# Kernel optimization log

Measured on AMD Instinct MI355X. Metric: run time of the kernel, lower is better.

Reference implementation:

```python
import jax, jax.numpy as jnp
import numpy as np

NUM_NODES = 100000
NUM_REL = 500
D = 400          # entity_out_dim[0] * nheads_GAT[0] = 200 * 2
C = 50           # conv_out_channels
B = 16384        # batch of triples


def setup_inputs() -> dict:
    key = jax.random.key(0)
    k = jax.random.split(key, 7)
    entity_emb = jax.random.normal(k[0], (NUM_NODES, D), jnp.float32)
    relation_emb = jax.random.normal(k[1], (NUM_REL, D), jnp.float32)
    # Conv2d(1, C, (1, 3)) weight: [C, 1, 1, 3]; xavier-ish scale
    conv_w = jax.random.normal(k[2], (C, 1, 1, 3), jnp.float32) * 0.5
    conv_b = jnp.zeros((C,), jnp.float32)
    # Linear(D*C, 1)
    fc_w = jax.random.normal(k[3], (1, D * C), jnp.float32) * 0.01
    fc_b = jnp.zeros((1,), jnp.float32)
    heads = jax.random.randint(k[4], (B,), 0, NUM_NODES)
    rels = jax.random.randint(k[5], (B,), 0, NUM_REL)
    tails = jax.random.randint(k[6], (B,), 0, NUM_NODES)
    batch_inputs = jnp.stack([heads, rels, tails], axis=1)  # [B, 3]
    return {
        "entity_emb": entity_emb,
        "relation_emb": relation_emb,
        "conv_w": conv_w,
        "conv_b": conv_b,
        "fc_w": fc_w,
        "fc_b": fc_b,
        "batch_inputs": batch_inputs,
    }


def reference(entity_emb, relation_emb, conv_w, conv_b, fc_w, fc_b, batch_inputs):
    # Gather (h, r, t) rows: irregular access into large tables
    h = entity_emb[batch_inputs[:, 0]]    # [B, D]
    r = relation_emb[batch_inputs[:, 1]]  # [B, D]
    t = entity_emb[batch_inputs[:, 2]]    # [B, D]
    # torch: cat -> [B, 3, D], transpose -> [B, D, 3], unsqueeze -> [B, 1, D, 3]
    x = jnp.stack([h, r, t], axis=-1)     # [B, D, 3]
    # Conv2d(1, C, (1, 3)): kernel spans full width -> per-channel dot over 3
    w = conv_w[:, 0, 0, :]                # [C, 3]
    out = jnp.einsum("bdk,ck->bcd", x, w) + conv_b[None, :, None]  # [B, C, D]
    out = jax.nn.relu(out)                # dropout is identity in eval mode
    # squeeze(-1).view(B, -1): channel-major flatten -> [B, C*D]
    flat = out.reshape(out.shape[0], -1)
    return flat @ fc_w.T + fc_b           # [B, 1]
```

## Files before the change

### kernel.cpp

```cpp
#include <hip/hip_runtime.h>


typedef _Float16 h2 __attribute__((ext_vector_type(2)));
typedef _Float16 h8 __attribute__((ext_vector_type(8)));

constexpr int D    = 400;
constexpr int CP   = 25;
constexpr int DPAD = 404;

static __device__ __forceinline__ float dot2acc(h2 a, h2 b, float c) {
#if __has_builtin(__builtin_amdgcn_fdot2)
    return __builtin_amdgcn_fdot2(a, b, c, false);
#else
    h2 p = a * b; return c + (float)p[0] + (float)p[1];
#endif
}
static __device__ __forceinline__ h2 dup(float v) {
    _Float16 x = (_Float16)v; h2 r; r[0] = x; r[1] = x; return r;
}

__global__ __attribute__((amdgpu_flat_work_group_size(512, 512), amdgpu_waves_per_eu(2, 4)))
void grcnet_pk16f(
    const float* __restrict__ entity_emb,
    const float* __restrict__ relation_emb,
    const float* __restrict__ conv_w,
    const float* __restrict__ conv_b,
    const float* __restrict__ fc_w,
    const float* __restrict__ fc_b,
    const int*   __restrict__ batch_inputs,
    float* __restrict__ out,
    int nB)
{
    __shared__ h2    fc_lds[CP][DPAD];
    __shared__ h2    conv_lds[CP][4];
    __shared__ float partials[2][4][4];

    const int tid  = threadIdx.x;
    const int lane = tid & 63;
    const int wv   = tid >> 6;
    const int grp  = wv >> 1;
    const int hc   = wv & 1;
    const int b0   = blockIdx.x * 16;
    if (b0 >= nB) return;

    const int bbase = __builtin_amdgcn_readfirstlane(b0 + 4 * grp);
    const int* bi = batch_inputs + 3 * bbase;
    const float* p0h = entity_emb   + (size_t)bi[0]  * D + lane;
    const float* p0r = relation_emb + (size_t)bi[1]  * D + lane;
    const float* p0t = entity_emb   + (size_t)bi[2]  * D + lane;
    const float* p1h = entity_emb   + (size_t)bi[3]  * D + lane;
    const float* p1r = relation_emb + (size_t)bi[4]  * D + lane;
    const float* p1t = entity_emb   + (size_t)bi[5]  * D + lane;
    const float* p2h = entity_emb   + (size_t)bi[6]  * D + lane;
    const float* p2r = relation_emb + (size_t)bi[7]  * D + lane;
    const float* p2t = entity_emb   + (size_t)bi[8]  * D + lane;
    const float* p3h = entity_emb   + (size_t)bi[9]  * D + lane;
    const float* p3r = relation_emb + (size_t)bi[10] * D + lane;
    const float* p3t = entity_emb   + (size_t)bi[11] * D + lane;

    const int  d6  = lane + 384;
    const bool a6  = (d6 < D);
    const int  i6  = a6 ? 384 : -lane;
    const h2*  fcb  = (const h2*)fc_lds + lane;
    const h2*  fcb6 = (const h2*)fc_lds + (a6 ? d6 : D);

    #define LOADI(S, IDX)                                                         \
        f##S##_0h = p0h[IDX]; f##S##_0r = p0r[IDX]; f##S##_0t = p0t[IDX];         \
        f##S##_1h = p1h[IDX]; f##S##_1r = p1r[IDX]; f##S##_1t = p1t[IDX];         \
        f##S##_2h = p2h[IDX]; f##S##_2r = p2r[IDX]; f##S##_2t = p2t[IDX];         \
        f##S##_3h = p3h[IDX]; f##S##_3r = p3r[IDX]; f##S##_3t = p3t[IDX];

    float fA_0h, fA_0r, fA_0t, fA_1h, fA_1r, fA_1t;
    float fA_2h, fA_2r, fA_2t, fA_3h, fA_3r, fA_3t;
    float fB_0h, fB_0r, fB_0t, fB_1h, fB_1r, fB_1t;
    float fB_2h, fB_2r, fB_2t, fB_3h, fB_3r, fB_3t;
    float fC_0h, fC_0r, fC_0t, fC_1h, fC_1r, fC_1t;
    float fC_2h, fC_2r, fC_2t, fC_3h, fC_3r, fC_3t;

    LOADI(A, 0)
    LOADI(B, 64)

    for (int k = tid; k < CP * 100; k += 512) {
        const int cp = k / 100;
        const int dq = k - cp * 100;
        const float4 A  = *(const float4*)(fc_w + (2*cp)     * D + 4*dq);
        const float4 Bv = *(const float4*)(fc_w + (2*cp + 1) * D + 4*dq);
        h8 g;
        g[0]=(_Float16)A.x; g[1]=(_Float16)Bv.x;
        g[2]=(_Float16)A.y; g[3]=(_Float16)Bv.y;
        g[4]=(_Float16)A.z; g[5]=(_Float16)Bv.z;
        g[6]=(_Float16)A.w; g[7]=(_Float16)Bv.w;
        *(h8*)&fc_lds[cp][4*dq] = g;
    }
    if (tid < CP * 4) {
        h2 z; z[0] = (_Float16)0; z[1] = (_Float16)0;
        fc_lds[tid >> 2][D + (tid & 3)] = z;
    }
    if (tid < CP) {
        const int c0 = 2 * tid;
        h2 wa, wb, wc, cb;
        wa[0]=(_Float16)conv_w[3*c0+0]; wa[1]=(_Float16)conv_w[3*c0+3];
        wb[0]=(_Float16)conv_w[3*c0+1]; wb[1]=(_Float16)conv_w[3*c0+4];
        wc[0]=(_Float16)conv_w[3*c0+2]; wc[1]=(_Float16)conv_w[3*c0+5];
        cb[0]=(_Float16)conv_b[c0];     cb[1]=(_Float16)conv_b[c0+1];
        conv_lds[tid][0]=wa; conv_lds[tid][1]=wb;
        conv_lds[tid][2]=wc; conv_lds[tid][3]=cb;
    }
    __syncthreads();

    float acc0 = 0.f, acc1 = 0.f, acc2 = 0.f, acc3 = 0.f;
    const h2 zero2 = (h2)(_Float16)0;

    #define COMPUTE(S, FB, FIDX0)                                                 \
    {                                                                             \
        const h2 H0 = dup(f##S##_0h), R0 = dup(f##S##_0r), T0 = dup(f##S##_0t);   \
        const h2 H1 = dup(f##S##_1h), R1 = dup(f##S##_1r), T1 = dup(f##S##_1t);   \
        const h2 H2 = dup(f##S##_2h), R2 = dup(f##S##_2r), T2 = dup(f##S##_2t);   \
        const h2 H3 = dup(f##S##_3h), R3 = dup(f##S##_3r), T3 = dup(f##S##_3t);   \
        _Pragma("unroll")                                                         \
        for (int j = 0; j < NC; ++j) {                                            \
            const h2 f2 = (FB)[(FIDX0) + (C0 + j) * DPAD];        \
            h2 s0 = H0*cwa[j] + (R0*cwb[j] + (T0*cwc[j] + ccb[j]));               \
            h2 s1 = H1*cwa[j] + (R1*cwb[j] + (T1*cwc[j] + ccb[j]));               \
            h2 s2 = H2*cwa[j] + (R2*cwb[j] + (T2*cwc[j] + ccb[j]));               \
            h2 s3 = H3*cwa[j] + (R3*cwb[j] + (T3*cwc[j] + ccb[j]));               \
            s0 = __builtin_elementwise_max(s0, zero2);                            \
            s1 = __builtin_elementwise_max(s1, zero2);                            \
            s2 = __builtin_elementwise_max(s2, zero2);                            \
            s3 = __builtin_elementwise_max(s3, zero2);                            \
            acc0 = dot2acc(s0, f2, acc0);                                         \
            acc1 = dot2acc(s1, f2, acc1);                                         \
            acc2 = dot2acc(s2, f2, acc2);                                         \
            acc3 = dot2acc(s3, f2, acc3);                                         \
        }                                                                         \
    }

    #define BODY(C0_, NC_)                                                        \
    {                                                                             \
        constexpr int C0 = (C0_), NC = (NC_);                                     \
        h2 cwa[NC], cwb[NC], cwc[NC], ccb[NC];                                    \
        _Pragma("unroll")                                                         \
        for (int j = 0; j < NC; ++j) {                                            \
            cwa[j] = conv_lds[C0+j][0]; cwb[j] = conv_lds[C0+j][1];               \
            cwc[j] = conv_lds[C0+j][2]; ccb[j] = conv_lds[C0+j][3];               \
        }                                                                         \
        LOADI(C, 128)  COMPUTE(A, fcb, 0*64)                                      \
        LOADI(A, 192)  COMPUTE(B, fcb, 1*64)                                      \
        LOADI(B, 256)  COMPUTE(C, fcb, 2*64)                                      \
        LOADI(C, 320)  COMPUTE(A, fcb, 3*64)                                      \
        LOADI(A, i6)   COMPUTE(B, fcb, 4*64)                                      \
                       COMPUTE(C, fcb, 5*64)                                      \
                       COMPUTE(A, fcb6, 0)                                        \
    }

    if (hc == 0) { BODY(0, 13) } else { BODY(13, 12) }
    #undef BODY
    #undef COMPUTE
    #undef LOADI

    #pragma unroll
    for (int off = 32; off > 0; off >>= 1) {
        acc0 += __shfl_xor(acc0, off);
        acc1 += __shfl_xor(acc1, off);
        acc2 += __shfl_xor(acc2, off);
        acc3 += __shfl_xor(acc3, off);
    }
    if (lane == 0) {
        partials[hc][grp][0] = acc0; partials[hc][grp][1] = acc1;
        partials[hc][grp][2] = acc2; partials[hc][grp][3] = acc3;
    }
    __syncthreads();

    if (tid < 16) {
        const int g = tid >> 2, j = tid & 3;
        out[b0 + 4*g + j] = partials[0][g][j] + partials[1][g][j] + fc_b[0];
    }
}

extern "C" void kernel_launch(void* const* d_in, const int* in_sizes, int n_in,
                              void* d_out, int out_size, void* d_ws, size_t ws_size,
                              hipStream_t stream) {
    const float* entity_emb   = (const float*)d_in[0];
    const float* relation_emb = (const float*)d_in[1];
    const float* conv_w       = (const float*)d_in[2];
    const float* conv_b       = (const float*)d_in[3];
    const float* fc_w         = (const float*)d_in[4];
    const float* fc_b         = (const float*)d_in[5];
    const int*   batch_inputs = (const int*)d_in[6];
    float* out = (float*)d_out;

    const int nB = in_sizes[6] / 3;
    const int blocks = (nB + 15) / 16;
    grcnet_pk16f<<<blocks, 512, 0, stream>>>(
        entity_emb, relation_emb, conv_w, conv_b, fc_w, fc_b, batch_inputs, out, nB);
}
```

Measured before the change: 47.38 us.

## Process two 16-triple groups per block to amortize fc_w LDS staging

Each block now handles 32 triples in two sequential groups of 16, so the fc_w half-precision staging into LDS and the conv weight loads are paid once per 32 triples instead of once per 16. The channel split is made uniform (13 and 13) by adding a zeroed padding channel, which lets both wave halves share one code path with runtime offsets. The row gathers move from three rotating register buffers to two. The trade-offs are half as many blocks for hiding gather latency, some redundant global loads in the loop prologue, and possible extra register pressure.

```diff
diff --git a/kernel.cpp b/kernel.cpp
--- a/kernel.cpp
+++ b/kernel.cpp
@@ -20,7 +20,7 @@
 }
 
 __global__ __attribute__((amdgpu_flat_work_group_size(512, 512), amdgpu_waves_per_eu(2, 4)))
-void grcnet_pk16f(
+void grcnet_pk16g(
     const float* __restrict__ entity_emb,
     const float* __restrict__ relation_emb,
     const float* __restrict__ conv_w,
@@ -31,38 +31,38 @@
     float* __restrict__ out,
     int nB)
 {
-    __shared__ h2    fc_lds[CP][DPAD];
-    __shared__ h2    conv_lds[CP][4];
-    __shared__ float partials[2][4][4];
+    __shared__ h2    fc_lds[CP + 1][DPAD];
+    __shared__ h2    conv_lds[CP + 1][4];
+    __shared__ float partials[2][2][4][4];
 
     const int tid  = threadIdx.x;
     const int lane = tid & 63;
     const int wv   = tid >> 6;
     const int grp  = wv >> 1;
     const int hc   = wv & 1;
-    const int b0   = blockIdx.x * 16;
-    if (b0 >= nB) return;
-
-    const int bbase = __builtin_amdgcn_readfirstlane(b0 + 4 * grp);
-    const int* bi = batch_inputs + 3 * bbase;
-    const float* p0h = entity_emb   + (size_t)bi[0]  * D + lane;
-    const float* p0r = relation_emb + (size_t)bi[1]  * D + lane;
-    const float* p0t = entity_emb   + (size_t)bi[2]  * D + lane;
-    const float* p1h = entity_emb   + (size_t)bi[3]  * D + lane;
-    const float* p1r = relation_emb + (size_t)bi[4]  * D + lane;
-    const float* p1t = entity_emb   + (size_t)bi[5]  * D + lane;
-    const float* p2h = entity_emb   + (size_t)bi[6]  * D + lane;
-    const float* p2r = relation_emb + (size_t)bi[7]  * D + lane;
-    const float* p2t = entity_emb   + (size_t)bi[8]  * D + lane;
-    const float* p3h = entity_emb   + (size_t)bi[9]  * D + lane;
-    const float* p3r = relation_emb + (size_t)bi[10] * D + lane;
-    const float* p3t = entity_emb   + (size_t)bi[11] * D + lane;
-
-    const int  d6  = lane + 384;
-    const bool a6  = (d6 < D);
-    const int  i6  = a6 ? 384 : -lane;
-    const h2*  fcb  = (const h2*)fc_lds + lane;
-    const h2*  fcb6 = (const h2*)fc_lds + (a6 ? d6 : D);
+    const int bq   = blockIdx.x * 32;
+    if (bq >= nB) return;
+
+    const float *p0h, *p0r, *p0t, *p1h, *p1r, *p1t;
+    const float *p2h, *p2r, *p2t, *p3h, *p3r, *p3t;
+
+    #define SETPTRS(B0)                                                           \
+    {                                                                             \
+        const int bbase = __builtin_amdgcn_readfirstlane((B0) + 4 * grp);         \
+        const int* bi = batch_inputs + 3 * bbase;                                 \
+        p0h = entity_emb   + (size_t)bi[0]  * D + lane;                           \
+        p0r = relation_emb + (size_t)bi[1]  * D + lane;                           \
+        p0t = entity_emb   + (size_t)bi[2]  * D + lane;                           \
+        p1h = entity_emb   + (size_t)bi[3]  * D + lane;                           \
+        p1r = relation_emb + (size_t)bi[4]  * D + lane;                           \
+        p1t = entity_emb   + (size_t)bi[5]  * D + lane;                           \
+        p2h = entity_emb   + (size_t)bi[6]  * D + lane;                           \
+        p2r = relation_emb + (size_t)bi[7]  * D + lane;                           \
+        p2t = entity_emb   + (size_t)bi[8]  * D + lane;                           \
+        p3h = entity_emb   + (size_t)bi[9]  * D + lane;                           \
+        p3r = relation_emb + (size_t)bi[10] * D + lane;                           \
+        p3t = entity_emb   + (size_t)bi[11] * D + lane;                           \
+    }
 
     #define LOADI(S, IDX)                                                         \
         f##S##_0h = p0h[IDX]; f##S##_0r = p0r[IDX]; f##S##_0t = p0t[IDX];         \
@@ -74,9 +74,8 @@
     float fA_2h, fA_2r, fA_2t, fA_3h, fA_3r, fA_3t;
     float fB_0h, fB_0r, fB_0t, fB_1h, fB_1r, fB_1t;
     float fB_2h, fB_2r, fB_2t, fB_3h, fB_3r, fB_3t;
-    float fC_0h, fC_0r, fC_0t, fC_1h, fC_1r, fC_1t;
-    float fC_2h, fC_2r, fC_2t, fC_3h, fC_3r, fC_3t;
-
+
+    SETPTRS(bq)
     LOADI(A, 0)
     LOADI(B, 64)
 
@@ -92,12 +91,14 @@
         g[6]=(_Float16)A.w; g[7]=(_Float16)Bv.w;
         *(h8*)&fc_lds[cp][4*dq] = g;
     }
-    if (tid < CP * 4) {
+    {
         h2 z; z[0] = (_Float16)0; z[1] = (_Float16)0;
-        fc_lds[tid >> 2][D + (tid & 3)] = z;
-    }
-    if (tid < CP) {
-        const int c0 = 2 * tid;
+        if (tid < CP * 4) fc_lds[tid >> 2][D + (tid & 3)] = z;
+        if (tid >= 64 && tid < 64 + DPAD) fc_lds[CP][tid - 64] = z;
+    }
+    if (tid < CP + 1) {
+        const int src = (tid == CP) ? (CP - 1) : tid;
+        const int c0 = 2 * src;
         h2 wa, wb, wc, cb;
         wa[0]=(_Float16)conv_w[3*c0+0]; wa[1]=(_Float16)conv_w[3*c0+3];
         wb[0]=(_Float16)conv_w[3*c0+1]; wb[1]=(_Float16)conv_w[3*c0+4];
@@ -108,7 +109,21 @@
     }
     __syncthreads();
 
-    float acc0 = 0.f, acc1 = 0.f, acc2 = 0.f, acc3 = 0.f;
+    const int C0 = 13 * hc;
+    constexpr int NC = 13;
+    h2 cwa[NC], cwb[NC], cwc[NC], ccb[NC];
+    #pragma unroll
+    for (int j = 0; j < NC; ++j) {
+        cwa[j] = conv_lds[C0+j][0]; cwb[j] = conv_lds[C0+j][1];
+        cwc[j] = conv_lds[C0+j][2]; ccb[j] = conv_lds[C0+j][3];
+    }
+
+    const int  d6 = lane + 384;
+    const bool a6 = (d6 < D);
+    const int  i6 = a6 ? 384 : -lane;
+    const h2* fcb  = &fc_lds[0][0] + C0 * DPAD + lane;
+    const h2* fcb6 = &fc_lds[0][0] + C0 * DPAD + (a6 ? d6 : D);
+
     const h2 zero2 = (h2)(_Float16)0;
 
     #define COMPUTE(S, FB, FIDX0)                                                 \
@@ -119,7 +134,7 @@
         const h2 H3 = dup(f##S##_3h), R3 = dup(f##S##_3r), T3 = dup(f##S##_3t);   \
         _Pragma("unroll")                                                         \
         for (int j = 0; j < NC; ++j) {                                            \
-            const h2 f2 = (FB)[(FIDX0) + (C0 + j) * DPAD];        \
+            const h2 f2 = (FB)[(FIDX0) + j * DPAD];               \
             h2 s0 = H0*cwa[j] + (R0*cwb[j] + (T0*cwc[j] + ccb[j]));               \
             h2 s1 = H1*cwa[j] + (R1*cwb[j] + (T1*cwc[j] + ccb[j]));               \
             h2 s2 = H2*cwa[j] + (R2*cwb[j] + (T2*cwc[j] + ccb[j]));               \
@@ -135,45 +150,55 @@
         }                                                                         \
     }
 
-    #define BODY(C0_, NC_)                                                        \
-    {                                                                             \
-        constexpr int C0 = (C0_), NC = (NC_);                                     \
-        h2 cwa[NC], cwb[NC], cwc[NC], ccb[NC];                                    \
-        _Pragma("unroll")                                                         \
-        for (int j = 0; j < NC; ++j) {                                            \
-            cwa[j] = conv_lds[C0+j][0]; cwb[j] = conv_lds[C0+j][1];               \
-            cwc[j] = conv_lds[C0+j][2]; ccb[j] = conv_lds[C0+j][3];               \
-        }                                                                         \
-        LOADI(C, 128)  COMPUTE(A, fcb, 0*64)                                      \
-        LOADI(A, 192)  COMPUTE(B, fcb, 1*64)                                      \
-        LOADI(B, 256)  COMPUTE(C, fcb, 2*64)                                      \
-        LOADI(C, 320)  COMPUTE(A, fcb, 3*64)                                      \
-        LOADI(A, i6)   COMPUTE(B, fcb, 4*64)                                      \
-                       COMPUTE(C, fcb, 5*64)                                      \
-                       COMPUTE(A, fcb6, 0)                                        \
-    }
-
-    if (hc == 0) { BODY(0, 13) } else { BODY(13, 12) }
-    #undef BODY
+    #pragma unroll 1
+    for (int g = 0; g < 2; ++g) {
+        const int b0 = bq + 16 * g;
+        if (b0 >= nB) break;
+        if (g) {
+            SETPTRS(b0)
+            LOADI(A, 0)
+            LOADI(B, 64)
+        }
+        float acc0 = 0.f, acc1 = 0.f, acc2 = 0.f, acc3 = 0.f;
+
+        LOADI(A, 128)
+        (void)0;
+        acc0 = 0.f; acc1 = 0.f; acc2 = 0.f; acc3 = 0.f;
+        if (g) { LOADI(A, 0) LOADI(B, 64) }
+        else   { LOADI(A, 0) LOADI(B, 64) }
+
+        COMPUTE(A, fcb, 0*64)   LOADI(A, 128)
+        COMPUTE(B, fcb, 1*64)   LOADI(B, 192)
+        COMPUTE(A, fcb, 2*64)   LOADI(A, 256)
+        COMPUTE(B, fcb, 3*64)   LOADI(B, 320)
+        COMPUTE(A, fcb, 4*64)   LOADI(A, i6)
+        COMPUTE(B, fcb, 5*64)
+        COMPUTE(A, fcb6, 0)
+
+        #pragma unroll
+        for (int off = 32; off > 0; off >>= 1) {
+            acc0 += __shfl_xor(acc0, off);
+            acc1 += __shfl_xor(acc1, off);
+            acc2 += __shfl_xor(acc2, off);
+            acc3 += __shfl_xor(acc3, off);
+        }
+        if (lane == 0) {
+            partials[g][hc][grp][0] = acc0; partials[g][hc][grp][1] = acc1;
+            partials[g][hc][grp][2] = acc2; partials[g][hc][grp][3] = acc3;
+        }
+    }
     #undef COMPUTE
     #undef LOADI
-
-    #pragma unroll
-    for (int off = 32; off > 0; off >>= 1) {
-        acc0 += __shfl_xor(acc0, off);
-        acc1 += __shfl_xor(acc1, off);
-        acc2 += __shfl_xor(acc2, off);
-        acc3 += __shfl_xor(acc3, off);
-    }
-    if (lane == 0) {
-        partials[hc][grp][0] = acc0; partials[hc][grp][1] = acc1;
-        partials[hc][grp][2] = acc2; partials[hc][grp][3] = acc3;
-    }
+    #undef SETPTRS
+
     __syncthreads();
 
-    if (tid < 16) {
-        const int g = tid >> 2, j = tid & 3;
-        out[b0 + 4*g + j] = partials[0][g][j] + partials[1][g][j] + fc_b[0];
+    if (tid < 32) {
+        const int g = tid >> 4, idx = tid & 15;
+        const int gr = idx >> 2, j = idx & 3;
+        const int b = bq + 16 * g + 4 * gr + j;
+        if (b < nB)
+            out[b] = partials[g][0][gr][j] + partials[g][1][gr][j] + fc_b[0];
     }
 }
 
@@ -190,7 +215,7 @@
     float* out = (float*)d_out;
 
     const int nB = in_sizes[6] / 3;
-    const int blocks = (nB + 15) / 16;
-    grcnet_pk16f<<<blocks, 512, 0, stream>>>(
+    const int blocks = (nB + 31) / 32;
+    grcnet_pk16g<<<blocks, 512, 0, stream>>>(
         entity_emb, relation_emb, conv_w, conv_b, fc_w, fc_b, batch_inputs, out, nB);
 }
```

Result: faster. 44.87 us (-5.3%).
